# Kernel tuning notes

Hardware: AMD Instinct MI355X
Metric: run time of the kernel (lower is better)

## Reference

```python
import jax, jax.numpy as jnp
import numpy as np

B, S, D = 1, 2048, 2048
H, KV, HD = 32, 8, 64          # heads, kv heads, head_dim
WINDOW = 1024                  # sliding window (left), causal
ROPE_THETA = 10000.0


def setup_inputs() -> dict:
    key = jax.random.key(0)
    ks = jax.random.split(key, 5)
    scale = 1.0 / np.sqrt(D)
    x = jax.random.normal(ks[0], (B, S, D), dtype=jnp.float32)
    wq = jax.random.normal(ks[1], (D, H * HD), dtype=jnp.float32) * scale
    wk = jax.random.normal(ks[2], (D, KV * HD), dtype=jnp.float32) * scale
    wv = jax.random.normal(ks[3], (D, KV * HD), dtype=jnp.float32) * scale
    wo = jax.random.normal(ks[4], (H * HD, D), dtype=jnp.float32) * scale
    # RoPE frequencies: freqs_cis = exp(i * t * theta^{-2j/hd}), stored as cos/sin
    inv_freq = 1.0 / (ROPE_THETA ** (np.arange(0, HD, 2, dtype=np.float32) / HD))  # [HD/2]
    t = np.arange(S, dtype=np.float32)
    ang = np.outer(t, inv_freq)  # [S, HD/2]
    freqs_cos = jnp.asarray(np.cos(ang), dtype=jnp.float32)
    freqs_sin = jnp.asarray(np.sin(ang), dtype=jnp.float32)
    return {"x": x, "wq": wq, "wk": wk, "wv": wv, "wo": wo,
            "freqs_cos": freqs_cos, "freqs_sin": freqs_sin}


def _apply_rope(t, cos, sin):
    # t: [B,S,h,HD]; pairs (t[...,2i], t[...,2i+1]) form complex numbers
    tr = t.reshape(*t.shape[:-1], HD // 2, 2)
    a, b = tr[..., 0], tr[..., 1]
    c = cos[None, :, None, :]  # [1,S,1,HD/2]
    s = sin[None, :, None, :]
    ra = a * c - b * s
    rb = a * s + b * c
    return jnp.stack([ra, rb], axis=-1).reshape(t.shape)


def reference(x, wq, wk, wv, wo, freqs_cos, freqs_sin):
    q = (x @ wq).reshape(B, S, H, HD)
    k = (x @ wk).reshape(B, S, KV, HD)
    v = (x @ wv).reshape(B, S, KV, HD)
    q = _apply_rope(q, freqs_cos, freqs_sin)
    k = _apply_rope(k, freqs_cos, freqs_sin)
    # GQA: repeat kv heads to match query heads
    k = jnp.repeat(k, H // KV, axis=2)  # [B,S,H,HD]
    v = jnp.repeat(v, H // KV, axis=2)
    scale = jnp.asarray(1.0 / np.sqrt(HD), dtype=x.dtype)
    scores = jnp.einsum('bqhd,bkhd->bhqk', q, k) * scale  # [B,H,S,S]
    i = jnp.arange(S)[:, None]
    j = jnp.arange(S)[None, :]
    allowed = (j <= i) & (j >= i - WINDOW)  # causal + sliding window
    scores = jnp.where(allowed[None, None], scores, jnp.asarray(-1e30, dtype=scores.dtype))
    attn = jax.nn.softmax(scores, axis=-1)
    out = jnp.einsum('bhqk,bkhd->bqhd', attn, v).reshape(B, S, H * HD)
    return out @ wo
```

## Files before the change

kernel.cpp:

```cpp
#include <hip/hip_runtime.h>
#include <stdint.h>

typedef __bf16 bf16_t;
typedef __bf16 bf16x8 __attribute__((ext_vector_type(8)));
typedef __bf16 bf16x4 __attribute__((ext_vector_type(4)));
typedef float floatx4 __attribute__((ext_vector_type(4)));

#define AS3(p) ((__attribute__((address_space(3))) void*)(p))
#define AS1(p) ((__attribute__((address_space(1))) void*)(void*)(p))

__global__ __launch_bounds__(256) void cvt_k(const float* __restrict__ src,
                                             bf16_t* __restrict__ dst, int n) {
  const int i = (blockIdx.x * 256 + threadIdx.x) * 8;
  if (i + 8 <= n) {
    floatx4 a = *(const floatx4*)&src[i];
    floatx4 b = *(const floatx4*)&src[i + 4];
    bf16x8 o;
#pragma unroll
    for (int j = 0; j < 4; ++j) { o[j] = (bf16_t)a[j]; o[4 + j] = (bf16_t)b[j]; }
    *(bf16x8*)&dst[i] = o;
  }
}

__global__ __launch_bounds__(256) void tr_k(const float* __restrict__ src, int ncols,
                                            bf16_t* __restrict__ dst) {
  __shared__ __align__(16) bf16_t T[64][68];
  const int t = threadIdx.x;
  const int nt = blockIdx.x * 64, kt = blockIdx.y * 64;
  const int r0 = t >> 4;
  const int c0 = (t & 15) << 2;
#pragma unroll
  for (int p = 0; p < 4; ++p) {
    const int row = p * 16 + r0;
    floatx4 v = *(const floatx4*)&src[(size_t)(kt + row) * ncols + nt + c0];
    bf16x4 b;
#pragma unroll
    for (int i = 0; i < 4; ++i) b[i] = (bf16_t)v[i];
    *(bf16x4*)&T[row][c0] = b;
  }
  __syncthreads();
#pragma unroll
  for (int p = 0; p < 4; ++p) {
    const int n = p * 16 + r0;
    bf16x4 tmp;
#pragma unroll
    for (int i = 0; i < 4; ++i) tmp[i] = T[c0 + i][n];
    *(bf16x4*)&dst[(size_t)(nt + n) * 2048 + kt + c0] = tmp;
  }
}

template <int EPI>
__global__ __launch_bounds__(256) void gemm_k(const bf16_t* __restrict__ A,
                                              const bf16_t* __restrict__ Bt,
                                              bf16_t* __restrict__ o0,
                                              bf16_t* __restrict__ o1,
                                              bf16_t* __restrict__ o2,
                                              float* __restrict__ fo,
                                              const float* __restrict__ fcos,
                                              const float* __restrict__ fsin) {
  constexpr int K = 2048;
  __shared__ __align__(16) bf16_t As[64 * 64];
  __shared__ __align__(16) bf16_t Bs[128 * 64];
  const int tid = threadIdx.x;
  const int lane = tid & 63;
  const int w = tid >> 6;
  const int quad = lane >> 4;
  const int l15 = lane & 15;
  const int m0 = blockIdx.y * 64;
  const int n0 = blockIdx.x * 128;
  const int sr = lane >> 3;
  const int sc = ((lane & 7) ^ (sr & 7)) << 3;
  const bf16_t* gA = A + (size_t)(m0 + w * 16 + sr) * K + sc;
  const bf16_t* gB = Bt + (size_t)(n0 + w * 32 + sr) * K + sc;
  bf16_t* lA = &As[w * 1024];
  bf16_t* lB = &Bs[w * 2048];
  floatx4 acc[4][2] = {};

  for (int k0 = 0; k0 < K; k0 += 64) {
    __builtin_amdgcn_global_load_lds(AS1(gA + k0), AS3(lA), 16, 0, 0);
    __builtin_amdgcn_global_load_lds(AS1(gA + 8 * K + k0), AS3(lA + 512), 16, 0, 0);
#pragma unroll
    for (int qq = 0; qq < 4; ++qq)
      __builtin_amdgcn_global_load_lds(AS1(gB + (size_t)qq * 8 * K + k0),
                                       AS3(lB + qq * 512), 16, 0, 0);
    __syncthreads();
#pragma unroll
    for (int kk = 0; kk < 2; ++kk) {
      const int co = ((kk * 4 + quad) ^ (l15 & 7)) << 3;
      bf16x8 af[4], bfr[2];
#pragma unroll
      for (int i = 0; i < 4; ++i) af[i] = *(const bf16x8*)&As[(i * 16 + l15) * 64 + co];
#pragma unroll
      for (int i = 0; i < 2; ++i)
        bfr[i] = *(const bf16x8*)&Bs[(w * 32 + i * 16 + l15) * 64 + co];
#pragma unroll
      for (int mi = 0; mi < 4; ++mi)
#pragma unroll
        for (int ni = 0; ni < 2; ++ni)
          acc[mi][ni] =
              __builtin_amdgcn_mfma_f32_16x16x32_bf16(af[mi], bfr[ni], acc[mi][ni], 0, 0, 0);
    }
    __syncthreads();
  }

  if constexpr (EPI == 0) {
#pragma unroll
    for (int ni = 0; ni < 2; ++ni) {
      const int col = n0 + w * 32 + ni * 16 + l15;
#pragma unroll
      for (int mi = 0; mi < 4; ++mi) {
        const int sb = m0 + mi * 16 + quad * 4;
        if (col < 2560) {
          const int fi = (col & 63) >> 1;
#pragma unroll
          for (int r = 0; r < 4; ++r) {
            const float v = acc[mi][ni][r];
            const float prt = __shfl_xor(v, 1);
            const int s = sb + r;
            const float c = fcos[s * 32 + fi];
            const float sn = fsin[s * 32 + fi];
            const float ov = (col & 1) ? (prt * sn + v * c) : (v * c - prt * sn);
            if (col < 2048)
              o0[(size_t)s * 2048 + col] = (bf16_t)ov;
            else
              o1[(size_t)s * 512 + (col - 2048)] = (bf16_t)ov;
          }
        } else {
          const int sp = (sb & ~31) | (quad * 8 + (mi & 1) * 4);
          bf16x4 pv;
#pragma unroll
          for (int r = 0; r < 4; ++r) pv[r] = (bf16_t)acc[mi][ni][r];
          *(bf16x4*)&o2[(size_t)(col - 2560) * 2048 + sp] = pv;
        }
      }
    }
  } else {
#pragma unroll
    for (int ni = 0; ni < 2; ++ni) {
      const int col = n0 + w * 32 + ni * 16 + l15;
#pragma unroll
      for (int mi = 0; mi < 4; ++mi) {
        const int sb = m0 + mi * 16 + quad * 4;
#pragma unroll
        for (int r = 0; r < 4; ++r) fo[(size_t)(sb + r) * 2048 + col] = acc[mi][ni][r];
      }
    }
  }
}

__global__ __launch_bounds__(256) void attn_k(const bf16_t* __restrict__ qb_,
                                              const bf16_t* __restrict__ kb_,
                                              const bf16_t* __restrict__ vt_,
                                              bf16_t* __restrict__ ob_) {
  __shared__ __align__(16) bf16_t sm[2][8 * 512];
  const int lane = threadIdx.x & 63, w = threadIdx.x >> 6;
  const int quad = lane >> 4, l15 = lane & 15;
  const int h = blockIdx.y, g = h >> 2;
  const int qb = (gridDim.x - 1 - blockIdx.x) * 64;
  const int qw = qb + w * 16;
  const int q = qw + l15;
  const bf16_t* qrow = qb_ + (size_t)q * 2048 + h * 64;
  const bf16x8 qf0 = *(const bf16x8*)(qrow + quad * 8);
  const bf16x8 qf1 = *(const bf16x8*)(qrow + 32 + quad * 8);
  floatx4 acc0 = {}, acc1 = {}, acc2 = {}, acc3 = {}, accl = {};
  const float SC = 0.125f * 1.44269504088896340736f;
  bf16x8 ones;
#pragma unroll
  for (int i = 0; i < 8; ++i) ones[i] = (bf16_t)1.0f;

  int kbB = qb - 1024;
  if (kbB < 0) kbB = 0;
  kbB &= ~31;
  const int nT = (qb + 64 - kbB) >> 5;
  int myS = qw - 1024;
  if (myS < 0) myS = 0;
  myS &= ~31;
  const int myE = qw + 16;

  const int lr = lane & 15, lc = lane >> 4;
  const bf16_t* gk = kb_ + (size_t)(kbB + (w >> 1) * 16 + lr) * 512 + g * 64 +
                     ((w & 1) * 4 + lc) * 8;
  const bf16_t* gv = vt_ + (size_t)(g * 64 + w * 16 + lr) * 2048 + kbB + lc * 8;

#define STAGE(bi, ti)                                                              \
  do {                                                                             \
    __builtin_amdgcn_global_load_lds(AS1(gk + (size_t)(ti) * (32 * 512)),          \
                                     AS3(&sm[bi][w * 512]), 16, 0, 0);             \
    __builtin_amdgcn_global_load_lds(AS1(gv + (size_t)(ti) * 32),                  \
                                     AS3(&sm[bi][(4 + w) * 512]), 16, 0, 0);       \
  } while (0)

#define MSK(pv, key)                                        \
  do {                                                      \
    if ((key) > q || (key) + 1024 < q) pv = -1.0e30f;       \
  } while (0)

  int kb = kbB;
  STAGE(0, 0);
  __syncthreads();
  for (int i = 0; i < nT; ++i, kb += 32) {
    if (i + 1 < nT) STAGE((i + 1) & 1, i + 1);
    if (kb >= myS && kb < myE) {
      const bf16_t* base = &sm[i & 1][(size_t)lane * 8];
      const bf16x8 k0 = *(const bf16x8*)(base);
      const bf16x8 k1 = *(const bf16x8*)(base + 512);
      const bf16x8 k2 = *(const bf16x8*)(base + 1024);
      const bf16x8 k3 = *(const bf16x8*)(base + 1536);
      const bf16x8 v0 = *(const bf16x8*)(base + 2048);
      const bf16x8 v1 = *(const bf16x8*)(base + 2560);
      const bf16x8 v2 = *(const bf16x8*)(base + 3072);
      const bf16x8 v3 = *(const bf16x8*)(base + 3584);
      floatx4 z0 = {}, z1 = {};
      z0 = __builtin_amdgcn_mfma_f32_16x16x32_bf16(k0, qf0, z0, 0, 0, 0);
      z0 = __builtin_amdgcn_mfma_f32_16x16x32_bf16(k1, qf1, z0, 0, 0, 0);
      z1 = __builtin_amdgcn_mfma_f32_16x16x32_bf16(k2, qf0, z1, 0, 0, 0);
      z1 = __builtin_amdgcn_mfma_f32_16x16x32_bf16(k3, qf1, z1, 0, 0, 0);
      float p0 = z0[0] * SC - 32.0f, p1 = z0[1] * SC - 32.0f;
      float p2 = z0[2] * SC - 32.0f, p3 = z0[3] * SC - 32.0f;
      float p4 = z1[0] * SC - 32.0f, p5 = z1[1] * SC - 32.0f;
      float p6 = z1[2] * SC - 32.0f, p7 = z1[3] * SC - 32.0f;
      if ((kb + 31 > qw) || (kb < qw - 1009)) {
        const int kq = kb + quad * 4;
        MSK(p0, kq + 0); MSK(p1, kq + 1); MSK(p2, kq + 2); MSK(p3, kq + 3);
        MSK(p4, kq + 16); MSK(p5, kq + 17); MSK(p6, kq + 18); MSK(p7, kq + 19);
      }
      bf16x8 pf;
      pf[0] = (bf16_t)__builtin_amdgcn_exp2f(p0);
      pf[1] = (bf16_t)__builtin_amdgcn_exp2f(p1);
      pf[2] = (bf16_t)__builtin_amdgcn_exp2f(p2);
      pf[3] = (bf16_t)__builtin_amdgcn_exp2f(p3);
      pf[4] = (bf16_t)__builtin_amdgcn_exp2f(p4);
      pf[5] = (bf16_t)__builtin_amdgcn_exp2f(p5);
      pf[6] = (bf16_t)__builtin_amdgcn_exp2f(p6);
      pf[7] = (bf16_t)__builtin_amdgcn_exp2f(p7);
      accl = __builtin_amdgcn_mfma_f32_16x16x32_bf16(ones, pf, accl, 0, 0, 0);
      acc0 = __builtin_amdgcn_mfma_f32_16x16x32_bf16(v0, pf, acc0, 0, 0, 0);
      acc1 = __builtin_amdgcn_mfma_f32_16x16x32_bf16(v1, pf, acc1, 0, 0, 0);
      acc2 = __builtin_amdgcn_mfma_f32_16x16x32_bf16(v2, pf, acc2, 0, 0, 0);
      acc3 = __builtin_amdgcn_mfma_f32_16x16x32_bf16(v3, pf, acc3, 0, 0, 0);
    }
    __syncthreads();
  }
#undef STAGE
#undef MSK

  const float inv = 1.0f / accl[0];
  bf16_t* obase = ob_ + (size_t)q * 2048 + h * 64 + quad * 4;
  bf16x4 ov;
#pragma unroll
  for (int r = 0; r < 4; ++r) ov[r] = (bf16_t)(acc0[r] * inv);
  *(bf16x4*)(obase) = ov;
#pragma unroll
  for (int r = 0; r < 4; ++r) ov[r] = (bf16_t)(acc1[r] * inv);
  *(bf16x4*)(obase + 16) = ov;
#pragma unroll
  for (int r = 0; r < 4; ++r) ov[r] = (bf16_t)(acc2[r] * inv);
  *(bf16x4*)(obase + 32) = ov;
#pragma unroll
  for (int r = 0; r < 4; ++r) ov[r] = (bf16_t)(acc3[r] * inv);
  *(bf16x4*)(obase + 48) = ov;
}

extern "C" void kernel_launch(void* const* d_in, const int* in_sizes, int n_in, void* d_out,
                              int out_size, void* d_ws, size_t ws_size, hipStream_t stream) {
  (void)in_sizes;
  (void)n_in;
  (void)out_size;
  (void)ws_size;
  const float* x = (const float*)d_in[0];
  const float* wq = (const float*)d_in[1];
  const float* wk = (const float*)d_in[2];
  const float* wv = (const float*)d_in[3];
  const float* wo = (const float*)d_in[4];
  const float* fcos = (const float*)d_in[5];
  const float* fsin = (const float*)d_in[6];
  float* out = (float*)d_out;

  bf16_t* xb = (bf16_t*)d_ws;
  bf16_t* wt = xb + (size_t)2048 * 2048;
  bf16_t* qbuf = wt + (size_t)5120 * 2048;
  bf16_t* kbuf = qbuf + (size_t)2048 * 2048;
  bf16_t* vtb = kbuf + (size_t)2048 * 512;
  bf16_t* att = vtb + (size_t)512 * 2048;

  cvt_k<<<2048, 256, 0, stream>>>(x, xb, 2048 * 2048);
  tr_k<<<dim3(32, 32), 256, 0, stream>>>(wq, 2048, wt);
  tr_k<<<dim3(8, 32), 256, 0, stream>>>(wk, 512, wt + (size_t)2048 * 2048);
  tr_k<<<dim3(8, 32), 256, 0, stream>>>(wv, 512, wt + (size_t)2560 * 2048);
  tr_k<<<dim3(32, 32), 256, 0, stream>>>(wo, 2048, wt + (size_t)3072 * 2048);
  gemm_k<0><<<dim3(24, 32), 256, 0, stream>>>(xb, wt, qbuf, kbuf, vtb, nullptr, fcos, fsin);
  attn_k<<<dim3(32, 32), 256, 0, stream>>>(qbuf, kbuf, vtb, att);
  gemm_k<1><<<dim3(16, 32), 256, 0, stream>>>(att, wt + (size_t)3072 * 2048, nullptr, nullptr,
                                              nullptr, out, fcos, fsin);
}
```

Before: 214.7 us.

## Merge prep kernels into one launch and double-buffer GEMM LDS tiles

The five conversion and transpose launches (x cast plus four weight transposes) are merged into a single prep kernel that dispatches on block index, removing four kernel launches and their tail gaps. The GEMM main loop gains two LDS buffers per operand, so the next K-tile's global-to-LDS load is issued before computing on the current tile. This overlaps memory latency with MFMA work, at the cost of doubling shared memory per block, which may lower occupancy.

```diff
diff --git a/kernel.cpp b/kernel.cpp
--- a/kernel.cpp
+++ b/kernel.cpp
@@ -9,34 +9,53 @@
 #define AS3(p) ((__attribute__((address_space(3))) void*)(p))
 #define AS1(p) ((__attribute__((address_space(1))) void*)(void*)(p))
 
-__global__ __launch_bounds__(256) void cvt_k(const float* __restrict__ src,
-                                             bf16_t* __restrict__ dst, int n) {
-  const int i = (blockIdx.x * 256 + threadIdx.x) * 8;
-  if (i + 8 <= n) {
-    floatx4 a = *(const floatx4*)&src[i];
-    floatx4 b = *(const floatx4*)&src[i + 4];
+__global__ __launch_bounds__(256) void prep_k(const float* __restrict__ x,
+                                              const float* __restrict__ wq,
+                                              const float* __restrict__ wk,
+                                              const float* __restrict__ wv,
+                                              const float* __restrict__ wo,
+                                              bf16_t* __restrict__ xb,
+                                              bf16_t* __restrict__ wt) {
+  __shared__ __align__(16) bf16_t T[64][68];
+  const int b = blockIdx.x;
+  const int t = threadIdx.x;
+  if (b < 2048) {
+    const int i = (b * 256 + t) * 8;
+    floatx4 a = *(const floatx4*)&x[i];
+    floatx4 c = *(const floatx4*)&x[i + 4];
     bf16x8 o;
 #pragma unroll
-    for (int j = 0; j < 4; ++j) { o[j] = (bf16_t)a[j]; o[4 + j] = (bf16_t)b[j]; }
-    *(bf16x8*)&dst[i] = o;
-  }
-}
-
-__global__ __launch_bounds__(256) void tr_k(const float* __restrict__ src, int ncols,
-                                            bf16_t* __restrict__ dst) {
-  __shared__ __align__(16) bf16_t T[64][68];
-  const int t = threadIdx.x;
-  const int nt = blockIdx.x * 64, kt = blockIdx.y * 64;
+    for (int j = 0; j < 4; ++j) { o[j] = (bf16_t)a[j]; o[4 + j] = (bf16_t)c[j]; }
+    *(bf16x8*)&xb[i] = o;
+    return;
+  }
+  int b2 = b - 2048;
+  const float* src;
+  int ncols, bx, by;
+  bf16_t* dst;
+  if (b2 < 1024) {
+    src = wq; ncols = 2048; dst = wt; bx = b2 & 31; by = b2 >> 5;
+  } else if (b2 < 1280) {
+    const int i2 = b2 - 1024;
+    src = wk; ncols = 512; dst = wt + (size_t)2048 * 2048; bx = i2 & 7; by = i2 >> 3;
+  } else if (b2 < 1536) {
+    const int i2 = b2 - 1280;
+    src = wv; ncols = 512; dst = wt + (size_t)2560 * 2048; bx = i2 & 7; by = i2 >> 3;
+  } else {
+    const int i2 = b2 - 1536;
+    src = wo; ncols = 2048; dst = wt + (size_t)3072 * 2048; bx = i2 & 31; by = i2 >> 5;
+  }
+  const int nt = bx * 64, kt = by * 64;
   const int r0 = t >> 4;
   const int c0 = (t & 15) << 2;
 #pragma unroll
   for (int p = 0; p < 4; ++p) {
     const int row = p * 16 + r0;
     floatx4 v = *(const floatx4*)&src[(size_t)(kt + row) * ncols + nt + c0];
-    bf16x4 b;
-#pragma unroll
-    for (int i = 0; i < 4; ++i) b[i] = (bf16_t)v[i];
-    *(bf16x4*)&T[row][c0] = b;
+    bf16x4 bb;
+#pragma unroll
+    for (int i = 0; i < 4; ++i) bb[i] = (bf16_t)v[i];
+    *(bf16x4*)&T[row][c0] = bb;
   }
   __syncthreads();
 #pragma unroll
@@ -59,8 +78,8 @@
                                               const float* __restrict__ fcos,
                                               const float* __restrict__ fsin) {
   constexpr int K = 2048;
-  __shared__ __align__(16) bf16_t As[64 * 64];
-  __shared__ __align__(16) bf16_t Bs[128 * 64];
+  __shared__ __align__(16) bf16_t As[2][64 * 64];
+  __shared__ __align__(16) bf16_t Bs[2][128 * 64];
   const int tid = threadIdx.x;
   const int lane = tid & 63;
   const int w = tid >> 6;
@@ -72,36 +91,46 @@
   const int sc = ((lane & 7) ^ (sr & 7)) << 3;
   const bf16_t* gA = A + (size_t)(m0 + w * 16 + sr) * K + sc;
   const bf16_t* gB = Bt + (size_t)(n0 + w * 32 + sr) * K + sc;
-  bf16_t* lA = &As[w * 1024];
-  bf16_t* lB = &Bs[w * 2048];
   floatx4 acc[4][2] = {};
 
-  for (int k0 = 0; k0 < K; k0 += 64) {
-    __builtin_amdgcn_global_load_lds(AS1(gA + k0), AS3(lA), 16, 0, 0);
-    __builtin_amdgcn_global_load_lds(AS1(gA + 8 * K + k0), AS3(lA + 512), 16, 0, 0);
-#pragma unroll
-    for (int qq = 0; qq < 4; ++qq)
-      __builtin_amdgcn_global_load_lds(AS1(gB + (size_t)qq * 8 * K + k0),
-                                       AS3(lB + qq * 512), 16, 0, 0);
+#define GSTAGE(buf, k0)                                                                    \
+  do {                                                                                     \
+    __builtin_amdgcn_global_load_lds(AS1(gA + (k0)), AS3(&As[buf][w * 1024]), 16, 0, 0);   \
+    __builtin_amdgcn_global_load_lds(AS1(gA + 8 * K + (k0)),                               \
+                                     AS3(&As[buf][w * 1024 + 512]), 16, 0, 0);             \
+    _Pragma("unroll") for (int qq = 0; qq < 4; ++qq)                                       \
+        __builtin_amdgcn_global_load_lds(AS1(gB + (size_t)qq * 8 * K + (k0)),              \
+                                         AS3(&Bs[buf][w * 2048 + qq * 512]), 16, 0, 0);    \
+  } while (0)
+
+#define GCOMPUTE(buf)                                                                      \
+  do {                                                                                     \
+    _Pragma("unroll") for (int kk = 0; kk < 2; ++kk) {                                     \
+      const int co = ((kk * 4 + quad) ^ (l15 & 7)) << 3;                                   \
+      bf16x8 af[4], bfr[2];                                                                \
+      _Pragma("unroll") for (int i = 0; i < 4; ++i) af[i] =                                \
+          *(const bf16x8*)&As[buf][(i * 16 + l15) * 64 + co];                              \
+      _Pragma("unroll") for (int i = 0; i < 2; ++i) bfr[i] =                               \
+          *(const bf16x8*)&Bs[buf][(w * 32 + i * 16 + l15) * 64 + co];                     \
+      _Pragma("unroll") for (int mi = 0; mi < 4; ++mi)                                     \
+          _Pragma("unroll") for (int ni = 0; ni < 2; ++ni) acc[mi][ni] =                   \
+              __builtin_amdgcn_mfma_f32_16x16x32_bf16(af[mi], bfr[ni], acc[mi][ni], 0, 0,  \
+                                                      0);                                  \
+    }                                                                                      \
+  } while (0)
+
+  GSTAGE(0, 0);
+  __syncthreads();
+  for (int k0 = 0; k0 < K; k0 += 128) {
+    GSTAGE(1, k0 + 64);
+    GCOMPUTE(0);
     __syncthreads();
-#pragma unroll
-    for (int kk = 0; kk < 2; ++kk) {
-      const int co = ((kk * 4 + quad) ^ (l15 & 7)) << 3;
-      bf16x8 af[4], bfr[2];
-#pragma unroll
-      for (int i = 0; i < 4; ++i) af[i] = *(const bf16x8*)&As[(i * 16 + l15) * 64 + co];
-#pragma unroll
-      for (int i = 0; i < 2; ++i)
-        bfr[i] = *(const bf16x8*)&Bs[(w * 32 + i * 16 + l15) * 64 + co];
-#pragma unroll
-      for (int mi = 0; mi < 4; ++mi)
-#pragma unroll
-        for (int ni = 0; ni < 2; ++ni)
-          acc[mi][ni] =
-              __builtin_amdgcn_mfma_f32_16x16x32_bf16(af[mi], bfr[ni], acc[mi][ni], 0, 0, 0);
-    }
+    if (k0 + 128 < K) GSTAGE(0, k0 + 128);
+    GCOMPUTE(1);
     __syncthreads();
   }
+#undef GSTAGE
+#undef GCOMPUTE
 
   if constexpr (EPI == 0) {
 #pragma unroll
@@ -283,11 +312,7 @@
   bf16_t* vtb = kbuf + (size_t)2048 * 512;
   bf16_t* att = vtb + (size_t)512 * 2048;
 
-  cvt_k<<<2048, 256, 0, stream>>>(x, xb, 2048 * 2048);
-  tr_k<<<dim3(32, 32), 256, 0, stream>>>(wq, 2048, wt);
-  tr_k<<<dim3(8, 32), 256, 0, stream>>>(wk, 512, wt + (size_t)2048 * 2048);
-  tr_k<<<dim3(8, 32), 256, 0, stream>>>(wv, 512, wt + (size_t)2560 * 2048);
-  tr_k<<<dim3(32, 32), 256, 0, stream>>>(wo, 2048, wt + (size_t)3072 * 2048);
+  prep_k<<<4608, 256, 0, stream>>>(x, wq, wk, wv, wo, xb, wt);
   gemm_k<0><<<dim3(24, 32), 256, 0, stream>>>(xb, wt, qbuf, kbuf, vtb, nullptr, fcos, fsin);
   attn_k<<<dim3(32, 32), 256, 0, stream>>>(qbuf, kbuf, vtb, att);
   gemm_k<1><<<dim3(16, 32), 256, 0, stream>>>(att, wt + (size_t)3072 * 2048, nullptr, nullptr,
```

Measured after the change: 206.8 us. -3.6%, faster.
